# Performance work log

Measured on AMD Instinct MI355X. Metric: run time of the kernel, lower is better.

The kernel has to match this reference:

```python
import jax, jax.numpy as jnp
import numpy as np

B, T, D, H = 1024, 128, 128, 8
HS = D // H  # 16, matches the hard-coded 16**-0.5 scale
EPS = 1e-5


def setup_inputs() -> dict:
    key = jax.random.key(0)
    ks = jax.random.split(key, 12)
    s = 0.02
    return {
        "x": jax.random.normal(ks[0], (B, T, D), jnp.float32),
        "Wq": jax.random.normal(ks[1], (H, D, HS), jnp.float32) * s,
        "Wk": jax.random.normal(ks[2], (H, D, HS), jnp.float32) * s,
        "Wv": jax.random.normal(ks[3], (H, D, HS), jnp.float32) * s,
        "Wo": jax.random.normal(ks[4], (D, D), jnp.float32) * s,
        "bo": jnp.zeros((D,), jnp.float32),
        "W1": jax.random.normal(ks[5], (D, 4 * D), jnp.float32) * s,
        "b1": jnp.zeros((4 * D,), jnp.float32),
        "W2": jax.random.normal(ks[6], (4 * D, D), jnp.float32) * s,
        "b2": jnp.zeros((D,), jnp.float32),
        "g1": jnp.ones((D,), jnp.float32),
        "be1": jnp.zeros((D,), jnp.float32),
        "g2": jnp.ones((D,), jnp.float32),
        "be2": jnp.zeros((D,), jnp.float32),
    }


def _layernorm(x, g, b):
    mu = jnp.mean(x, axis=-1, keepdims=True)
    var = jnp.mean(jnp.square(x - mu), axis=-1, keepdims=True)
    return (x - mu) * jax.lax.rsqrt(var + EPS) * g + b


def _block(x, Wq, Wk, Wv, Wo, bo, W1, b1, W2, b2, g1, be1, g2, be2):
    h = _layernorm(x, g1, be1)
    q = jnp.einsum('btd,hde->bhte', h, Wq)
    k = jnp.einsum('btd,hde->bhte', h, Wk)
    v = jnp.einsum('btd,hde->bhte', h, Wv)
    scores = jnp.einsum('bhte,bhse->bhts', q, k) * (16.0 ** -0.5)
    causal = jnp.tril(jnp.ones((T, T), bool))
    scores = jnp.where(causal, scores, -jnp.inf)
    wei = jax.nn.softmax(scores, axis=-1)  # dropout off (eval)
    o = jnp.einsum('bhts,bhse->bhte', wei, v)
    o = jnp.transpose(o, (0, 2, 1, 3)).reshape(x.shape[0], T, D)  # concat heads
    x = x + (o @ Wo + bo)
    h2 = _layernorm(x, g2, be2)
    ff = jax.nn.relu(h2 @ W1 + b1) @ W2 + b2
    return x + ff


def reference(x, Wq, Wk, Wv, Wo, bo, W1, b1, W2, b2, g1, be1, g2, be2):
    return _block(x, Wq, Wk, Wv, Wo, bo, W1, b1, W2, b2, g1, be1, g2, be2)
```

## Files before the change

kernel.cpp:

```cpp
#include <hip/hip_runtime.h>
#include <hip/hip_bf16.h>

typedef unsigned short u16;
typedef unsigned int u32;
typedef __bf16 bf16x8 __attribute__((ext_vector_type(8)));
typedef float f32x4 __attribute__((ext_vector_type(4)));

#define LDA 136

__device__ __forceinline__ u16 f2b(float f) {
  __bf16 b = (__bf16)f;
  return __builtin_bit_cast(u16, b);
}
__device__ __forceinline__ float b2f(u16 h) {
  u32 u = ((u32)h) << 16;
  return __builtin_bit_cast(float, u);
}
__device__ __forceinline__ u32 pk2(float lo, float hi) {
  return (u32)f2b(lo) | ((u32)f2b(hi) << 16);
}
__device__ __forceinline__ bf16x8 zero8() {
  union { int4 i; bf16x8 v; } u;
  u.i = make_int4(0, 0, 0, 0);
  return u.v;
}
__device__ __forceinline__ f32x4 mfma16(bf16x8 a, bf16x8 b, f32x4 c) {
  return __builtin_amdgcn_mfma_f32_16x16x32_bf16(a, b, c, 0, 0, 0);
}
__device__ __forceinline__ ushort4 pk4(float a, float b, float c, float d) {
  ushort4 r; r.x = f2b(a); r.y = f2b(b); r.z = f2b(c); r.w = f2b(d);
  return r;
}

__device__ __forceinline__ bf16x8 gatherB(const f32x4& ve, const f32x4& vo,
                                          bool odd_valid, float scale,
                                          int l15, int lg) {
  u32 pe0 = pk2(ve[0] * scale, ve[1] * scale);
  u32 pe1 = pk2(ve[2] * scale, ve[3] * scale);
  u32 po0 = 0, po1 = 0;
  if (odd_valid) {
    po0 = pk2(vo[0] * scale, vo[1] * scale);
    po1 = pk2(vo[2] * scale, vo[3] * scale);
  }
  int s0 = ((lg & 1) * 2) * 16 + l15;
  u32 a0 = __shfl(pe0, s0),      a1 = __shfl(pe1, s0);
  u32 a2 = __shfl(pe0, s0 + 16), a3 = __shfl(pe1, s0 + 16);
  u32 b0 = __shfl(po0, s0),      b1 = __shfl(po1, s0);
  u32 b2 = __shfl(po0, s0 + 16), b3 = __shfl(po1, s0 + 16);
  union { u32 u[4]; bf16x8 v; } fr;
  bool lo = (lg < 2);
  fr.u[0] = lo ? a0 : b0; fr.u[1] = lo ? a1 : b1;
  fr.u[2] = lo ? a2 : b2; fr.u[3] = lo ? a3 : b3;
  return fr.v;
}

__global__ void prep_kernel(const float* __restrict__ Wq, const float* __restrict__ Wk,
                            const float* __restrict__ Wv, const float* __restrict__ Wo,
                            const float* __restrict__ W1, const float* __restrict__ W2,
                            u16* __restrict__ o) {
  int i = blockIdx.x * 256 + threadIdx.x;
  if (i >= 196608) return;
  float v;
  if (i < 49152) {
    int which = i >> 14, j = i & 16383;
    int n = j >> 7, k = j & 127;
    const float* W = (which == 0) ? Wq : (which == 1) ? Wk : Wv;
    v = W[((n >> 4) * 128 + k) * 16 + (n & 15)];
  } else if (i < 65536) {
    int j = i - 49152;
    v = Wo[(j & 127) * 128 + (j >> 7)];
  } else if (i < 131072) {
    int j = i - 65536;
    v = W1[(j & 127) * 512 + (j >> 7)];
  } else {
    int j = i - 131072;
    int c = j >> 9, n = j & 511;
    v = W2[n * 128 + c];
  }
  o[i] = f2b(v);
}

__global__ void __launch_bounds__(512, 4)
tblock_kernel(const float* __restrict__ xg, const u16* __restrict__ wts,
              const float* __restrict__ bo, const float* __restrict__ b1,
              const float* __restrict__ b2, const float* __restrict__ g1,
              const float* __restrict__ be1, const float* __restrict__ g2,
              const float* __restrict__ be2, float* __restrict__ out) {
  extern __shared__ u16 sm[];
  u16* buf1 = sm;
  u16* buf2 = sm + 128 * LDA;

  const int tid  = threadIdx.x;
  const int w    = tid >> 6;
  const int lane = tid & 63;
  const int l15  = lane & 15;
  const int lg   = lane >> 4;
  const int mr   = w >> 2;
  const int nc   = w & 3;
  const int tr0  = mr * 64;
  const int cb   = nc * 32;

  const u16* WqT  = wts;
  const u16* WkT  = wts + 16384;
  const u16* WvT  = wts + 32768;
  const u16* WoT  = wts + 49152;
  const u16* W1T  = wts + 65536;
  const u16* W2T2 = wts + 131072;

  const float* xp = xg + (size_t)blockIdx.x * 16384;
  float*       op = out + (size_t)blockIdx.x * 16384;

  const f32x4 zf4 = {0.f, 0.f, 0.f, 0.f};
  const bf16x8 zb8 = zero8();

  {
    const int t = w * 16 + l15;
    float v[8][4];
    #pragma unroll
    for (int nt = 0; nt < 8; ++nt) {
      float4 f = *(const float4*)(xp + t * 128 + nt * 16 + lg * 4);
      v[nt][0] = f.x; v[nt][1] = f.y; v[nt][2] = f.z; v[nt][3] = f.w;
    }
    float s = 0.f;
    #pragma unroll
    for (int nt = 0; nt < 8; ++nt)
      #pragma unroll
      for (int r = 0; r < 4; ++r) s += v[nt][r];
    s += __shfl_xor(s, 16); s += __shfl_xor(s, 32);
    float mu = s * 0.0078125f;
    float vv = 0.f;
    #pragma unroll
    for (int nt = 0; nt < 8; ++nt)
      #pragma unroll
      for (int r = 0; r < 4; ++r) { float d = v[nt][r] - mu; vv += d * d; }
    vv += __shfl_xor(vv, 16); vv += __shfl_xor(vv, 32);
    float rs = rsqrtf(vv * 0.0078125f + 1e-5f);
    #pragma unroll
    for (int nt = 0; nt < 8; ++nt) {
      float4 gv = *(const float4*)(g1 + nt * 16 + lg * 4);
      float4 bv = *(const float4*)(be1 + nt * 16 + lg * 4);
      *(ushort4*)(buf1 + t * LDA + nt * 16 + lg * 4) =
          pk4((v[nt][0] - mu) * rs * gv.x + bv.x, (v[nt][1] - mu) * rs * gv.y + bv.y,
              (v[nt][2] - mu) * rs * gv.z + bv.z, (v[nt][3] - mu) * rs * gv.w + bv.w);
    }
  }
  __syncthreads();

  bf16x8 av[4];
  {
    bf16x8 wv[4];
    #pragma unroll
    for (int kk = 0; kk < 4; ++kk)
      wv[kk] = *(const bf16x8*)(WvT + (w * 16 + l15) * 128 + kk * 32 + lg * 8);
    f32x4 vprev = zf4;
    #pragma unroll
    for (int mt = 0; mt < 8; ++mt) {
      f32x4 va = zf4;
      #pragma unroll
      for (int kk = 0; kk < 4; ++kk)
        va = mfma16(*(const bf16x8*)(buf1 + (mt * 16 + l15) * LDA + kk * 32 + lg * 8),
                    wv[kk], va);
      if (mt & 1) av[mt >> 1] = gatherB(vprev, va, true, 1.f, l15, lg);
      else        vprev = va;
    }
  }

  bf16x8 bk[8];
  {
    bf16x8 wk[4], wq[4];
    #pragma unroll
    for (int kk = 0; kk < 4; ++kk) {
      wk[kk] = *(const bf16x8*)(WkT + (w * 16 + l15) * 128 + kk * 32 + lg * 8);
      wq[kk] = *(const bf16x8*)(WqT + (w * 16 + l15) * 128 + kk * 32 + lg * 8);
    }
    u32 qp[8][2];
    #pragma unroll
    for (int mt = 0; mt < 8; ++mt) {
      bf16x8 hf[4];
      #pragma unroll
      for (int kk = 0; kk < 4; ++kk)
        hf[kk] = *(const bf16x8*)(buf1 + (mt * 16 + l15) * LDA + kk * 32 + lg * 8);
      f32x4 ka = zf4, qa = zf4;
      #pragma unroll
      for (int kk = 0; kk < 4; ++kk) {
        ka = mfma16(wk[kk], hf[kk], ka);
        qa = mfma16(wq[kk], hf[kk], qa);
      }
      *(ushort4*)(buf2 + (mt * 16 + l15) * LDA + w * 16 + lg * 4) =
          pk4(ka[0], ka[1], ka[2], ka[3]);
      qp[mt][0] = pk2(qa[0], qa[1]);
      qp[mt][1] = pk2(qa[2], qa[3]);
    }
    #pragma unroll
    for (int st = 0; st < 8; ++st) {
      bk[st] = zb8;
      if (lg < 2)
        bk[st] = *(const bf16x8*)(buf2 + (st * 16 + l15) * LDA + w * 16 + lg * 8);
    }
    #pragma unroll
    for (int mt = 0; mt < 8; ++mt) {
      union { u32 u[2]; ushort4 s; } uq;
      uq.u[0] = qp[mt][0]; uq.u[1] = qp[mt][1];
      *(ushort4*)(buf2 + (mt * 16 + l15) * LDA + w * 16 + lg * 4) = uq.s;
    }
  }

  #pragma unroll 1
  for (int mt = 0; mt < 8; ++mt) {
    bf16x8 aq = zb8;
    if (lg < 2)
      aq = *(const bf16x8*)(buf2 + (mt * 16 + l15) * LDA + w * 16 + lg * 8);

    f32x4 sacc[8];
    #pragma unroll
    for (int st = 0; st < 8; ++st)
      sacc[st] = (st <= mt) ? mfma16(bk[st], aq, zf4) : zf4;

    float mx = -3.0e38f;
    #pragma unroll
    for (int st = 0; st < 8; ++st) if (st <= mt) {
      #pragma unroll
      for (int rg = 0; rg < 4; ++rg) {
        float sv = sacc[st][rg] * 0.25f;
        bool ok = (st < mt) || ((lg * 4 + rg) <= l15);
        sv = ok ? sv : -1.0e30f;
        sacc[st][rg] = sv;
        mx = fmaxf(mx, sv);
      }
    }
    mx = fmaxf(mx, __shfl_xor(mx, 16));
    mx = fmaxf(mx, __shfl_xor(mx, 32));
    float sum = 0.f;
    #pragma unroll
    for (int st = 0; st < 8; ++st) if (st <= mt) {
      #pragma unroll
      for (int rg = 0; rg < 4; ++rg) {
        float e = __expf(sacc[st][rg] - mx);
        sacc[st][rg] = e;
        sum += e;
      }
    }
    sum += __shfl_xor(sum, 16);
    sum += __shfl_xor(sum, 32);
    float inv = 1.f / sum;

    f32x4 oa = zf4;
    #pragma unroll
    for (int kk = 0; kk < 4; ++kk) if (kk <= (mt >> 1)) {
      bf16x8 fr = gatherB(sacc[2 * kk], sacc[2 * kk + 1], (2 * kk + 1) <= mt, inv, l15, lg);
      oa = mfma16(av[kk], fr, oa);
    }
    *(ushort4*)(buf2 + (mt * 16 + l15) * LDA + w * 16 + lg * 4) =
        pk4(oa[0], oa[1], oa[2], oa[3]);
  }
  __syncthreads();

  f32x4 oacc[4][2];
  {
    bf16x8 wo[2][4];
    #pragma unroll
    for (int ct = 0; ct < 2; ++ct)
      #pragma unroll
      for (int kk = 0; kk < 4; ++kk)
        wo[ct][kk] = *(const bf16x8*)(WoT + (cb + ct * 16 + l15) * 128 + kk * 32 + lg * 8);
    #pragma unroll
    for (int mt = 0; mt < 4; ++mt) {
      const int t = tr0 + mt * 16 + l15;
      bf16x8 ofr[4];
      #pragma unroll
      for (int kk = 0; kk < 4; ++kk)
        ofr[kk] = *(const bf16x8*)(buf2 + t * LDA + kk * 32 + lg * 8);
      #pragma unroll
      for (int ct = 0; ct < 2; ++ct) {
        f32x4 acc = zf4;
        #pragma unroll
        for (int kk = 0; kk < 4; ++kk)
          acc = mfma16(wo[ct][kk], ofr[kk], acc);
        float4 xv  = *(const float4*)(xp + t * 128 + cb + ct * 16 + lg * 4);
        float4 bov = *(const float4*)(bo + cb + ct * 16 + lg * 4);
        float4 b2v = *(const float4*)(b2 + cb + ct * 16 + lg * 4);
        float x10 = acc[0] + bov.x + xv.x;
        float x11 = acc[1] + bov.y + xv.y;
        float x12 = acc[2] + bov.z + xv.z;
        float x13 = acc[3] + bov.w + xv.w;
        oacc[mt][ct][0] = x10 + b2v.x;
        oacc[mt][ct][1] = x11 + b2v.y;
        oacc[mt][ct][2] = x12 + b2v.z;
        oacc[mt][ct][3] = x13 + b2v.w;
        *(ushort4*)(buf1 + t * LDA + cb + ct * 16 + lg * 4) = pk4(x10, x11, x12, x13);
      }
    }
  }
  __syncthreads();

  {
    const int t = w * 16 + l15;
    float v[8][4];
    #pragma unroll
    for (int nt = 0; nt < 8; ++nt) {
      ushort4 u = *(const ushort4*)(buf1 + t * LDA + nt * 16 + lg * 4);
      v[nt][0] = b2f(u.x); v[nt][1] = b2f(u.y); v[nt][2] = b2f(u.z); v[nt][3] = b2f(u.w);
    }
    float s = 0.f;
    #pragma unroll
    for (int nt = 0; nt < 8; ++nt)
      #pragma unroll
      for (int r = 0; r < 4; ++r) s += v[nt][r];
    s += __shfl_xor(s, 16); s += __shfl_xor(s, 32);
    float mu = s * 0.0078125f;
    float vv = 0.f;
    #pragma unroll
    for (int nt = 0; nt < 8; ++nt)
      #pragma unroll
      for (int r = 0; r < 4; ++r) { float d = v[nt][r] - mu; vv += d * d; }
    vv += __shfl_xor(vv, 16); vv += __shfl_xor(vv, 32);
    float rs = rsqrtf(vv * 0.0078125f + 1e-5f);
    #pragma unroll
    for (int nt = 0; nt < 8; ++nt) {
      float4 gv = *(const float4*)(g2 + nt * 16 + lg * 4);
      float4 bv = *(const float4*)(be2 + nt * 16 + lg * 4);
      *(ushort4*)(buf1 + t * LDA + nt * 16 + lg * 4) =
          pk4((v[nt][0] - mu) * rs * gv.x + bv.x, (v[nt][1] - mu) * rs * gv.y + bv.y,
              (v[nt][2] - mu) * rs * gv.z + bv.z, (v[nt][3] - mu) * rs * gv.w + bv.w);
    }
  }
  __syncthreads();

  {
    #pragma unroll 1
    for (int cc = 0; cc < 4; ++cc) {
      bf16x8 w1f[2][4];
      #pragma unroll
      for (int ct = 0; ct < 2; ++ct)
        #pragma unroll
        for (int kk = 0; kk < 4; ++kk)
          w1f[ct][kk] = *(const bf16x8*)(W1T + (cc * 128 + cb + ct * 16 + l15) * 128 + kk * 32 + lg * 8);
      #pragma unroll
      for (int mt = 0; mt < 4; ++mt) {
        const int t = tr0 + mt * 16 + l15;
        bf16x8 h2f[4];
        #pragma unroll
        for (int kk = 0; kk < 4; ++kk)
          h2f[kk] = *(const bf16x8*)(buf1 + t * LDA + kk * 32 + lg * 8);
        #pragma unroll
        for (int ct = 0; ct < 2; ++ct) {
          f32x4 fa = zf4;
          #pragma unroll
          for (int kk = 0; kk < 4; ++kk)
            fa = mfma16(w1f[ct][kk], h2f[kk], fa);
          float4 bv = *(const float4*)(b1 + cc * 128 + cb + ct * 16 + lg * 4);
          *(ushort4*)(buf2 + t * LDA + cb + ct * 16 + lg * 4) =
              pk4(fmaxf(fa[0] + bv.x, 0.f), fmaxf(fa[1] + bv.y, 0.f),
                  fmaxf(fa[2] + bv.z, 0.f), fmaxf(fa[3] + bv.w, 0.f));
        }
      }
      __syncthreads();

      bf16x8 w2f[2][4];
      #pragma unroll
      for (int ct = 0; ct < 2; ++ct)
        #pragma unroll
        for (int kk = 0; kk < 4; ++kk)
          w2f[ct][kk] = *(const bf16x8*)(W2T2 + (cb + ct * 16 + l15) * 512 + cc * 128 + kk * 32 + lg * 8);
      #pragma unroll
      for (int mt = 0; mt < 4; ++mt) {
        bf16x8 rf[4];
        #pragma unroll
        for (int kk = 0; kk < 4; ++kk)
          rf[kk] = *(const bf16x8*)(buf2 + (tr0 + mt * 16 + l15) * LDA + kk * 32 + lg * 8);
        #pragma unroll
        for (int ct = 0; ct < 2; ++ct)
          #pragma unroll
          for (int kk = 0; kk < 4; ++kk)
            oacc[mt][ct] = mfma16(w2f[ct][kk], rf[kk], oacc[mt][ct]);
      }
      if (cc < 3) __syncthreads();
    }

    #pragma unroll
    for (int mt = 0; mt < 4; ++mt) {
      const int t = tr0 + mt * 16 + l15;
      #pragma unroll
      for (int ct = 0; ct < 2; ++ct) {
        float4 st;
        st.x = oacc[mt][ct][0];
        st.y = oacc[mt][ct][1];
        st.z = oacc[mt][ct][2];
        st.w = oacc[mt][ct][3];
        *(float4*)(op + t * 128 + cb + ct * 16 + lg * 4) = st;
      }
    }
  }
}

extern "C" void kernel_launch(void* const* d_in, const int* in_sizes, int n_in,
                              void* d_out, int out_size, void* d_ws, size_t ws_size,
                              hipStream_t stream) {
  const float* x   = (const float*)d_in[0];
  const float* Wq  = (const float*)d_in[1];
  const float* Wk  = (const float*)d_in[2];
  const float* Wv  = (const float*)d_in[3];
  const float* Wo  = (const float*)d_in[4];
  const float* bo  = (const float*)d_in[5];
  const float* W1  = (const float*)d_in[6];
  const float* b1  = (const float*)d_in[7];
  const float* W2  = (const float*)d_in[8];
  const float* b2  = (const float*)d_in[9];
  const float* g1  = (const float*)d_in[10];
  const float* be1 = (const float*)d_in[11];
  const float* g2  = (const float*)d_in[12];
  const float* be2 = (const float*)d_in[13];
  u16* wts = (u16*)d_ws;

  prep_kernel<<<768, 256, 0, stream>>>(Wq, Wk, Wv, Wo, W1, W2, wts);

  const int smem_bytes = 2 * 128 * LDA * 2;
  hipFuncSetAttribute(reinterpret_cast<const void*>(tblock_kernel),
                      hipFuncAttributeMaxDynamicSharedMemorySize, smem_bytes);
  tblock_kernel<<<1024, 512, smem_bytes, stream>>>(x, wts, bo, b1, b2, g1, be1, g2,
                                                   be2, (float*)d_out);
}
```

Measured before the change: 154.2 us.

## Shrink shared memory footprint to raise occupancy, keep K in registers via shuffles

```diff
diff --git a/kernel.cpp b/kernel.cpp
--- a/kernel.cpp
+++ b/kernel.cpp
@@ -7,6 +7,7 @@
 typedef float f32x4 __attribute__((ext_vector_type(4)));
 
 #define LDA 136
+#define LDR 72
 
 __device__ __forceinline__ u16 f2b(float f) {
   __bf16 b = (__bf16)f;
@@ -51,6 +52,19 @@
   bool lo = (lg < 2);
   fr.u[0] = lo ? a0 : b0; fr.u[1] = lo ? a1 : b1;
   fr.u[2] = lo ? a2 : b2; fr.u[3] = lo ? a3 : b3;
+  return fr.v;
+}
+
+__device__ __forceinline__ bf16x8 buildK(u32 k0, u32 k1, int l15, int lg) {
+  int lgc = lg & 1;
+  u32 r0 = __shfl(k0, (2 * lgc + 0) * 16 + l15);
+  u32 r1 = __shfl(k1, (2 * lgc + 0) * 16 + l15);
+  u32 r2 = __shfl(k0, (2 * lgc + 1) * 16 + l15);
+  u32 r3 = __shfl(k1, (2 * lgc + 1) * 16 + l15);
+  union { u32 u[4]; bf16x8 v; } fr;
+  bool lo = (lg < 2);
+  fr.u[0] = lo ? r0 : 0; fr.u[1] = lo ? r1 : 0;
+  fr.u[2] = lo ? r2 : 0; fr.u[3] = lo ? r3 : 0;
   return fr.v;
 }
 
@@ -80,7 +94,7 @@
   o[i] = f2b(v);
 }
 
-__global__ void __launch_bounds__(512, 4)
+__global__ void __launch_bounds__(512, 6)
 tblock_kernel(const float* __restrict__ xg, const u16* __restrict__ wts,
               const float* __restrict__ bo, const float* __restrict__ b1,
               const float* __restrict__ b2, const float* __restrict__ g1,
@@ -88,17 +102,16 @@
               const float* __restrict__ be2, float* __restrict__ out) {
   extern __shared__ u16 sm[];
   u16* buf1 = sm;
-  u16* buf2 = sm + 128 * LDA;
+  u16* bufr = sm + 128 * LDA;
 
   const int tid  = threadIdx.x;
   const int w    = tid >> 6;
   const int lane = tid & 63;
   const int l15  = lane & 15;
   const int lg   = lane >> 4;
-  const int mr   = w >> 2;
-  const int nc   = w & 3;
-  const int tr0  = mr * 64;
-  const int cb   = nc * 32;
+  const int tr0  = (w >> 2) * 64;
+  const int cb   = (w & 3) * 32;
+  const int cw   = w & 3;
 
   const u16* WqT  = wts;
   const u16* WkT  = wts + 16384;
@@ -165,56 +178,68 @@
     }
   }
 
-  bf16x8 bk[8];
-  {
-    bf16x8 wk[4], wq[4];
-    #pragma unroll
-    for (int kk = 0; kk < 4; ++kk) {
+  u32 kp[8][2];
+  {
+    bf16x8 wk[4];
+    #pragma unroll
+    for (int kk = 0; kk < 4; ++kk)
       wk[kk] = *(const bf16x8*)(WkT + (w * 16 + l15) * 128 + kk * 32 + lg * 8);
+    #pragma unroll
+    for (int st = 0; st < 8; ++st) {
+      f32x4 ka = zf4;
+      #pragma unroll
+      for (int kk = 0; kk < 4; ++kk)
+        ka = mfma16(wk[kk],
+                    *(const bf16x8*)(buf1 + (st * 16 + l15) * LDA + kk * 32 + lg * 8),
+                    ka);
+      kp[st][0] = pk2(ka[0], ka[1]);
+      kp[st][1] = pk2(ka[2], ka[3]);
+    }
+  }
+
+  u32 qp[8][2];
+  {
+    bf16x8 wq[4];
+    #pragma unroll
+    for (int kk = 0; kk < 4; ++kk)
       wq[kk] = *(const bf16x8*)(WqT + (w * 16 + l15) * 128 + kk * 32 + lg * 8);
-    }
-    u32 qp[8][2];
     #pragma unroll
     for (int mt = 0; mt < 8; ++mt) {
-      bf16x8 hf[4];
-      #pragma unroll
-      for (int kk = 0; kk < 4; ++kk)
-        hf[kk] = *(const bf16x8*)(buf1 + (mt * 16 + l15) * LDA + kk * 32 + lg * 8);
-      f32x4 ka = zf4, qa = zf4;
-      #pragma unroll
-      for (int kk = 0; kk < 4; ++kk) {
-        ka = mfma16(wk[kk], hf[kk], ka);
-        qa = mfma16(wq[kk], hf[kk], qa);
-      }
-      *(ushort4*)(buf2 + (mt * 16 + l15) * LDA + w * 16 + lg * 4) =
-          pk4(ka[0], ka[1], ka[2], ka[3]);
+      f32x4 qa = zf4;
+      #pragma unroll
+      for (int kk = 0; kk < 4; ++kk)
+        qa = mfma16(wq[kk],
+                    *(const bf16x8*)(buf1 + (mt * 16 + l15) * LDA + kk * 32 + lg * 8),
+                    qa);
       qp[mt][0] = pk2(qa[0], qa[1]);
       qp[mt][1] = pk2(qa[2], qa[3]);
     }
-    #pragma unroll
-    for (int st = 0; st < 8; ++st) {
-      bk[st] = zb8;
-      if (lg < 2)
-        bk[st] = *(const bf16x8*)(buf2 + (st * 16 + l15) * LDA + w * 16 + lg * 8);
-    }
-    #pragma unroll
-    for (int mt = 0; mt < 8; ++mt) {
-      union { u32 u[2]; ushort4 s; } uq;
-      uq.u[0] = qp[mt][0]; uq.u[1] = qp[mt][1];
-      *(ushort4*)(buf2 + (mt * 16 + l15) * LDA + w * 16 + lg * 4) = uq.s;
-    }
+  }
+  __syncthreads();
+
+  #pragma unroll
+  for (int mt = 0; mt < 8; ++mt) {
+    union { u32 u[2]; ushort4 s; } uq;
+    uq.u[0] = qp[mt][0]; uq.u[1] = qp[mt][1];
+    *(ushort4*)(buf1 + (mt * 16 + l15) * LDA + w * 16 + lg * 4) = uq.s;
   }
 
   #pragma unroll 1
   for (int mt = 0; mt < 8; ++mt) {
     bf16x8 aq = zb8;
     if (lg < 2)
-      aq = *(const bf16x8*)(buf2 + (mt * 16 + l15) * LDA + w * 16 + lg * 8);
+      aq = *(const bf16x8*)(buf1 + (mt * 16 + l15) * LDA + w * 16 + lg * 8);
 
     f32x4 sacc[8];
     #pragma unroll
-    for (int st = 0; st < 8; ++st)
-      sacc[st] = (st <= mt) ? mfma16(bk[st], aq, zf4) : zf4;
+    for (int st = 0; st < 8; ++st) {
+      if (st <= mt) {
+        bf16x8 bk = buildK(kp[st][0], kp[st][1], l15, lg);
+        sacc[st] = mfma16(bk, aq, zf4);
+      } else {
+        sacc[st] = zf4;
+      }
+    }
 
     float mx = -3.0e38f;
     #pragma unroll
@@ -250,7 +275,7 @@
       bf16x8 fr = gatherB(sacc[2 * kk], sacc[2 * kk + 1], (2 * kk + 1) <= mt, inv, l15, lg);
       oa = mfma16(av[kk], fr, oa);
     }
-    *(ushort4*)(buf2 + (mt * 16 + l15) * LDA + w * 16 + lg * 4) =
+    *(ushort4*)(buf1 + (mt * 16 + l15) * LDA + w * 16 + lg * 4) =
         pk4(oa[0], oa[1], oa[2], oa[3]);
   }
   __syncthreads();
@@ -269,7 +294,7 @@
       bf16x8 ofr[4];
       #pragma unroll
       for (int kk = 0; kk < 4; ++kk)
-        ofr[kk] = *(const bf16x8*)(buf2 + t * LDA + kk * 32 + lg * 8);
+        ofr[kk] = *(const bf16x8*)(buf1 + t * LDA + kk * 32 + lg * 8);
       #pragma unroll
       for (int ct = 0; ct < 2; ++ct) {
         f32x4 acc = zf4;
@@ -278,18 +303,22 @@
           acc = mfma16(wo[ct][kk], ofr[kk], acc);
         float4 xv  = *(const float4*)(xp + t * 128 + cb + ct * 16 + lg * 4);
         float4 bov = *(const float4*)(bo + cb + ct * 16 + lg * 4);
-        float4 b2v = *(const float4*)(b2 + cb + ct * 16 + lg * 4);
-        float x10 = acc[0] + bov.x + xv.x;
-        float x11 = acc[1] + bov.y + xv.y;
-        float x12 = acc[2] + bov.z + xv.z;
-        float x13 = acc[3] + bov.w + xv.w;
-        oacc[mt][ct][0] = x10 + b2v.x;
-        oacc[mt][ct][1] = x11 + b2v.y;
-        oacc[mt][ct][2] = x12 + b2v.z;
-        oacc[mt][ct][3] = x13 + b2v.w;
-        *(ushort4*)(buf1 + t * LDA + cb + ct * 16 + lg * 4) = pk4(x10, x11, x12, x13);
+        oacc[mt][ct][0] = acc[0] + bov.x + xv.x;
+        oacc[mt][ct][1] = acc[1] + bov.y + xv.y;
+        oacc[mt][ct][2] = acc[2] + bov.z + xv.z;
+        oacc[mt][ct][3] = acc[3] + bov.w + xv.w;
       }
     }
+  }
+  __syncthreads();
+
+  #pragma unroll
+  for (int mt = 0; mt < 4; ++mt) {
+    const int t = tr0 + mt * 16 + l15;
+    #pragma unroll
+    for (int ct = 0; ct < 2; ++ct)
+      *(ushort4*)(buf1 + t * LDA + cb + ct * 16 + lg * 4) =
+          pk4(oacc[mt][ct][0], oacc[mt][ct][1], oacc[mt][ct][2], oacc[mt][ct][3]);
   }
   __syncthreads();
 
@@ -326,69 +355,61 @@
   }
   __syncthreads();
 
-  {
-    #pragma unroll 1
-    for (int cc = 0; cc < 4; ++cc) {
-      bf16x8 w1f[2][4];
+  #pragma unroll 1
+  for (int c8 = 0; c8 < 8; ++c8) {
+    bf16x8 w1f[4];
+    #pragma unroll
+    for (int kk = 0; kk < 4; ++kk)
+      w1f[kk] = *(const bf16x8*)(W1T + (c8 * 64 + cw * 16 + l15) * 128 + kk * 32 + lg * 8);
+    float4 b1v = *(const float4*)(b1 + c8 * 64 + cw * 16 + lg * 4);
+    #pragma unroll
+    for (int tt = 0; tt < 4; ++tt) {
+      const int t = tr0 + tt * 16 + l15;
+      f32x4 fa = zf4;
+      #pragma unroll
+      for (int kk = 0; kk < 4; ++kk)
+        fa = mfma16(w1f[kk],
+                    *(const bf16x8*)(buf1 + t * LDA + kk * 32 + lg * 8), fa);
+      *(ushort4*)(bufr + t * LDR + cw * 16 + lg * 4) =
+          pk4(fmaxf(fa[0] + b1v.x, 0.f), fmaxf(fa[1] + b1v.y, 0.f),
+              fmaxf(fa[2] + b1v.z, 0.f), fmaxf(fa[3] + b1v.w, 0.f));
+    }
+    __syncthreads();
+
+    bf16x8 w2f[2][2];
+    #pragma unroll
+    for (int ct = 0; ct < 2; ++ct)
+      #pragma unroll
+      for (int kk = 0; kk < 2; ++kk)
+        w2f[ct][kk] = *(const bf16x8*)(W2T2 + (cb + ct * 16 + l15) * 512 + c8 * 64 + kk * 32 + lg * 8);
+    #pragma unroll
+    for (int mt = 0; mt < 4; ++mt) {
+      const int t = tr0 + mt * 16 + l15;
+      bf16x8 rf[2];
+      #pragma unroll
+      for (int kk = 0; kk < 2; ++kk)
+        rf[kk] = *(const bf16x8*)(bufr + t * LDR + kk * 32 + lg * 8);
       #pragma unroll
       for (int ct = 0; ct < 2; ++ct)
         #pragma unroll
-        for (int kk = 0; kk < 4; ++kk)
-          w1f[ct][kk] = *(const bf16x8*)(W1T + (cc * 128 + cb + ct * 16 + l15) * 128 + kk * 32 + lg * 8);
-      #pragma unroll
-      for (int mt = 0; mt < 4; ++mt) {
-        const int t = tr0 + mt * 16 + l15;
-        bf16x8 h2f[4];
-        #pragma unroll
-        for (int kk = 0; kk < 4; ++kk)
-          h2f[kk] = *(const bf16x8*)(buf1 + t * LDA + kk * 32 + lg * 8);
-        #pragma unroll
-        for (int ct = 0; ct < 2; ++ct) {
-          f32x4 fa = zf4;
-          #pragma unroll
-          for (int kk = 0; kk < 4; ++kk)
-            fa = mfma16(w1f[ct][kk], h2f[kk], fa);
-          float4 bv = *(const float4*)(b1 + cc * 128 + cb + ct * 16 + lg * 4);
-          *(ushort4*)(buf2 + t * LDA + cb + ct * 16 + lg * 4) =
-              pk4(fmaxf(fa[0] + bv.x, 0.f), fmaxf(fa[1] + bv.y, 0.f),
-                  fmaxf(fa[2] + bv.z, 0.f), fmaxf(fa[3] + bv.w, 0.f));
-        }
-      }
-      __syncthreads();
-
-      bf16x8 w2f[2][4];
-      #pragma unroll
-      for (int ct = 0; ct < 2; ++ct)
-        #pragma unroll
-        for (int kk = 0; kk < 4; ++kk)
-          w2f[ct][kk] = *(const bf16x8*)(W2T2 + (cb + ct * 16 + l15) * 512 + cc * 128 + kk * 32 + lg * 8);
-      #pragma unroll
-      for (int mt = 0; mt < 4; ++mt) {
-        bf16x8 rf[4];
-        #pragma unroll
-        for (int kk = 0; kk < 4; ++kk)
-          rf[kk] = *(const bf16x8*)(buf2 + (tr0 + mt * 16 + l15) * LDA + kk * 32 + lg * 8);
-        #pragma unroll
-        for (int ct = 0; ct < 2; ++ct)
-          #pragma unroll
-          for (int kk = 0; kk < 4; ++kk)
-            oacc[mt][ct] = mfma16(w2f[ct][kk], rf[kk], oacc[mt][ct]);
-      }
-      if (cc < 3) __syncthreads();
-    }
-
-    #pragma unroll
-    for (int mt = 0; mt < 4; ++mt) {
-      const int t = tr0 + mt * 16 + l15;
-      #pragma unroll
-      for (int ct = 0; ct < 2; ++ct) {
-        float4 st;
-        st.x = oacc[mt][ct][0];
-        st.y = oacc[mt][ct][1];
-        st.z = oacc[mt][ct][2];
-        st.w = oacc[mt][ct][3];
-        *(float4*)(op + t * 128 + cb + ct * 16 + lg * 4) = st;
-      }
+        for (int kk = 0; kk < 2; ++kk)
+          oacc[mt][ct] = mfma16(w2f[ct][kk], rf[kk], oacc[mt][ct]);
+    }
+    __syncthreads();
+  }
+
+  #pragma unroll
+  for (int mt = 0; mt < 4; ++mt) {
+    const int t = tr0 + mt * 16 + l15;
+    #pragma unroll
+    for (int ct = 0; ct < 2; ++ct) {
+      float4 b2v = *(const float4*)(b2 + cb + ct * 16 + lg * 4);
+      float4 st;
+      st.x = oacc[mt][ct][0] + b2v.x;
+      st.y = oacc[mt][ct][1] + b2v.y;
+      st.z = oacc[mt][ct][2] + b2v.z;
+      st.w = oacc[mt][ct][3] + b2v.w;
+      *(float4*)(op + t * 128 + cb + ct * 16 + lg * 4) = st;
     }
   }
 }
@@ -414,7 +435,7 @@
 
   prep_kernel<<<768, 256, 0, stream>>>(Wq, Wk, Wv, Wo, W1, W2, wts);
 
-  const int smem_bytes = 2 * 128 * LDA * 2;
+  const int smem_bytes = (128 * LDA + 128 * LDR) * 2;
   hipFuncSetAttribute(reinterpret_cast<const void*>(tblock_kernel),
                       hipFuncAttributeMaxDynamicSharedMemorySize, smem_bytes);
   tblock_kernel<<<1024, 512, smem_bytes, stream>>>(x, wts, bo, b1, b2, g1, be1, g2,
```

Result: slower. 359.9 us (+133.3%).
